# Optimization experiments

Measured on AMD Instinct MI355X. Metric: run time of the kernel, lower is better.

Reference implementation:

```python
import jax, jax.numpy as jnp
import numpy as np

G = 5          # conv groups / adjacency groups
EPS = 1e-5     # BatchNorm eps


def _bn(x, gamma, beta):
    # training-mode BatchNorm2d over (B, J, K) per channel, biased variance
    mean = jnp.mean(x, axis=(0, 2, 3), keepdims=True)
    var = jnp.mean((x - mean) ** 2, axis=(0, 2, 3), keepdims=True)
    xhat = (x - mean) * jax.lax.rsqrt(var + EPS)
    return xhat * gamma[None, :, None, None] + beta[None, :, None, None]


def _xavier(key, shape, fan_in, fan_out):
    a = np.sqrt(6.0 / (fan_in + fan_out))
    return jax.random.uniform(key, shape, jnp.float32, -a, a)


def setup_inputs() -> dict:
    key = jax.random.key(0)
    k0, k1, k2, k3 = jax.random.split(key, 4)
    B, Cin, J, K = 8, 320, 256, 62
    outc = 480
    cin_g, cout_g = Cin // G, outc // G   # 64, 96
    x = jax.random.normal(k0, (B, Cin, J, K), jnp.float32)
    L = jax.random.uniform(k1, (G, K, K), jnp.float32)
    # grouped 1x1 conv weights, stored per-group: [G, out_per_g, in_per_g]
    W1 = _xavier(k2, (G, cout_g, cin_g), cin_g, cout_g)
    W2 = _xavier(k3, (G, cout_g, cout_g), cout_g, cout_g)
    gamma1 = jnp.ones((outc,), jnp.float32)
    beta1 = jnp.zeros((outc,), jnp.float32)
    gamma2 = jnp.ones((outc,), jnp.float32)
    beta2 = jnp.zeros((outc,), jnp.float32)
    return {"x": x, "L": L, "W1": W1, "W2": W2,
            "gamma1": gamma1, "beta1": beta1,
            "gamma2": gamma2, "beta2": beta2}


def reference(x, L, W1, W2, gamma1, beta1, gamma2, beta2):
    B, Cin, J, K = x.shape
    cout_g = W1.shape[1]
    outc = G * cout_g
    # grouped 1x1 conv #1: [B,G,cin_g,J,K] x [G,cout_g,cin_g]
    xg = x.reshape(B, G, Cin // G, J, K)
    h = jnp.einsum('bgcjk,goc->bgojk', xg, W1).reshape(B, outc, J, K)
    h = jax.nn.elu(_bn(h, gamma1, beta1))
    # grouped 1x1 conv #2
    hg = h.reshape(B, G, cout_g, J, K)
    h2 = jnp.einsum('bgcjk,goc->bgojk', hg, W2).reshape(B, outc, J, K)
    h2 = _bn(h2, gamma2, beta2)
    # per-group adjacency einsum: split channels into G groups of cout_g
    y = jnp.einsum('bgijk,gkp->bgijp', h2.reshape(B, G, cout_g, J, K), L)
    return y.reshape(B, outc, J, K)
```

## Files before the change

### kernel.cpp

```cpp
#include <hip/hip_runtime.h>
#include <hip/hip_bf16.h>

#define G 5
#define B 8
#define CIN 320
#define CIN_G 64
#define COUT 480
#define COUT_G 96
#define NPOS 15872
#define NSTAT (B*NPOS)
#define BN_EPS 1e-5f
#define KDIM 62
#define SLABBF 31744

typedef float  f32x4 __attribute__((ext_vector_type(4)));
typedef float  f32x2 __attribute__((ext_vector_type(2)));
typedef __bf16 bf16x8 __attribute__((ext_vector_type(8)));
typedef __bf16 bf16x4 __attribute__((ext_vector_type(4)));

__global__ __launch_bounds__(256) void k_prep(
    const float* __restrict__ W1, const float* __restrict__ W2, const float* __restrict__ L,
    __bf16* __restrict__ W1b, __bf16* __restrict__ W2b, float* __restrict__ lcs)
{
    const int bx = blockIdx.x;
    if (bx < 300) {
        const int i = bx * 256 + threadIdx.x;
        if (i < 30720) W1b[i] = (__bf16)W1[i];
        else W2b[i - 30720] = (__bf16)W2[i - 30720];
    } else {
        const int g = bx - 300, p = threadIdx.x;
        if (p < 64) {
            float s = 0.f;
            if (p < KDIM)
                for (int k = 0; k < KDIM; ++k) s += L[(g * KDIM + k) * KDIM + p];
            lcs[g * 64 + p] = s;
        }
    }
}

__global__ __launch_bounds__(256) void k_stat1(
    const float* __restrict__ x, const __bf16* __restrict__ W1b,
    float* __restrict__ sum1, float* __restrict__ sq1)
{
    __shared__ __bf16 wl[COUT_G * 72];
    __shared__ float st[COUT_G * 2];
    const int b = blockIdx.z, g = blockIdx.y;
    for (int i = threadIdx.x; i < 768; i += 256) {
        const int idx = i * 8, o = idx >> 6, c = idx & 63;
        *(bf16x8*)&wl[o * 72 + c] = *(const bf16x8*)&W1b[g * 6144 + idx];
    }
    if (threadIdx.x < COUT_G * 2) st[threadIdx.x] = 0.f;
    __syncthreads();

    const int wid = threadIdx.x >> 6, lane = threadIdx.x & 63;
    const int lg = lane >> 4, lr = lane & 15;
    const int jw = blockIdx.x * 4 + wid;
    const float* xb = x + ((size_t)b * CIN + g * CIN_G) * NPOS;

    f32x4 acc1[6][4];
#pragma unroll
    for (int mt = 0; mt < 6; ++mt)
#pragma unroll
        for (int nt = 0; nt < 4; ++nt) acc1[mt][nt] = (f32x4){0.f,0.f,0.f,0.f};

#pragma unroll
    for (int ks = 0; ks < 2; ++ks) {
        const int c0 = ks * 32 + lg * 8;
        bf16x8 af[6];
#pragma unroll
        for (int mt = 0; mt < 6; ++mt)
            af[mt] = *(const bf16x8*)&wl[(mt * 16 + lr) * 72 + c0];
#pragma unroll
        for (int nt = 0; nt < 4; ++nt) {
            const int kcol = nt * 16 + lr;
            bf16x8 bfv;
            if (kcol < KDIM) {
                const float* xp = xb + jw * KDIM + kcol;
#pragma unroll
                for (int i = 0; i < 8; ++i) bfv[i] = (__bf16)xp[(size_t)(c0 + i) * NPOS];
            } else {
#pragma unroll
                for (int i = 0; i < 8; ++i) bfv[i] = (__bf16)0.f;
            }
#pragma unroll
            for (int mt = 0; mt < 6; ++mt)
                acc1[mt][nt] = __builtin_amdgcn_mfma_f32_16x16x32_bf16(af[mt], bfv, acc1[mt][nt], 0, 0, 0);
        }
    }

#pragma unroll
    for (int mt = 0; mt < 6; ++mt) {
#pragma unroll
        for (int r = 0; r < 4; ++r) {
            float s = 0.f, q = 0.f;
#pragma unroll
            for (int nt = 0; nt < 4; ++nt) {
                const float v = acc1[mt][nt][r];
                s += v; q += v * v;
            }
#pragma unroll
            for (int m = 1; m <= 8; m <<= 1) {
                s += __shfl_xor(s, m);
                q += __shfl_xor(q, m);
            }
            if (lr == 0) {
                atomicAdd(&st[(mt * 16 + lg * 4 + r) * 2], s);
                atomicAdd(&st[(mt * 16 + lg * 4 + r) * 2 + 1], q);
            }
        }
    }
    __syncthreads();
    if (threadIdx.x < COUT_G) {
        atomicAdd(&sum1[g * COUT_G + threadIdx.x], st[threadIdx.x * 2]);
        atomicAdd(&sq1[g * COUT_G + threadIdx.x], st[threadIdx.x * 2 + 1]);
    }
}

__global__ void k_fin(const float* __restrict__ sum, const float* __restrict__ sq,
                      const float* __restrict__ gamma, const float* __restrict__ beta,
                      float* __restrict__ a, float* __restrict__ bb)
{
    const int ch = blockIdx.x * blockDim.x + threadIdx.x;
    if (ch < COUT) {
        const float invN = 1.f / (float)NSTAT;
        const float mean = sum[ch] * invN;
        const float var  = sq[ch] * invN - mean * mean;
        const float rstd = rsqrtf(var + BN_EPS);
        const float av = gamma[ch] * rstd;
        a[ch]  = av;
        bb[ch] = beta[ch] - mean * av;
    }
}

__global__ __launch_bounds__(256, 2) void k_fused(
    const float* __restrict__ x, const __bf16* __restrict__ W1b, const __bf16* __restrict__ W2b,
    const float* __restrict__ a1, const float* __restrict__ b1,
    __bf16* __restrict__ h2b, float* __restrict__ sum2, float* __restrict__ sq2)
{
    __shared__ __bf16 wl[COUT_G * 72];
    __shared__ __bf16 ht[4 * 6144];
    __shared__ float a1l[96], b1l[96], st[192];
    const int b = blockIdx.z, g = blockIdx.y;
    for (int i = threadIdx.x; i < 768; i += 256) {
        const int idx = i * 8, o = idx >> 6, c = idx & 63;
        *(bf16x8*)&wl[o * 72 + c] = *(const bf16x8*)&W1b[g * 6144 + idx];
    }
    if (threadIdx.x < 96) {
        a1l[threadIdx.x] = a1[g * 96 + threadIdx.x];
        b1l[threadIdx.x] = b1[g * 96 + threadIdx.x];
    }
    if (threadIdx.x < 192) st[threadIdx.x] = 0.f;
    __syncthreads();

    const int wid = threadIdx.x >> 6, lane = threadIdx.x & 63;
    const int lg = lane >> 4, lr = lane & 15;
    const int jw = blockIdx.x * 4 + wid;
    const float* xb = x + ((size_t)b * CIN + g * CIN_G) * NPOS;
    char* htw = (char*)(ht + wid * 6144);

    {
        f32x4 acc1[6][4];
#pragma unroll
        for (int mt = 0; mt < 6; ++mt)
#pragma unroll
            for (int nt = 0; nt < 4; ++nt) acc1[mt][nt] = (f32x4){0.f,0.f,0.f,0.f};

#pragma unroll
        for (int ks = 0; ks < 2; ++ks) {
            const int c0 = ks * 32 + lg * 8;
            bf16x8 af[6];
#pragma unroll
            for (int mt = 0; mt < 6; ++mt)
                af[mt] = *(const bf16x8*)&wl[(mt * 16 + lr) * 72 + c0];
#pragma unroll
            for (int nt = 0; nt < 4; ++nt) {
                const int kcol = nt * 16 + lr;
                bf16x8 bfv;
                if (kcol < KDIM) {
                    const float* xp = xb + jw * KDIM + kcol;
#pragma unroll
                    for (int i = 0; i < 8; ++i) bfv[i] = (__bf16)xp[(size_t)(c0 + i) * NPOS];
                } else {
#pragma unroll
                    for (int i = 0; i < 8; ++i) bfv[i] = (__bf16)0.f;
                }
#pragma unroll
                for (int mt = 0; mt < 6; ++mt)
                    acc1[mt][nt] = __builtin_amdgcn_mfma_f32_16x16x32_bf16(af[mt], bfv, acc1[mt][nt], 0, 0, 0);
            }
        }
#pragma unroll
        for (int mt = 0; mt < 6; ++mt) {
            const int o0 = mt * 16 + lg * 4;
            const int c8 = o0 >> 3;
            const int half = (o0 & 7) >> 2;
#pragma unroll
            for (int nt = 0; nt < 4; ++nt) {
                const int pl = nt * 16 + lr;
                bf16x4 pv;
#pragma unroll
                for (int r = 0; r < 4; ++r) {
                    const int o = o0 + r;
                    float t = a1l[o] * acc1[mt][nt][r] + b1l[o];
                    t = t > 0.f ? t : (__expf(t) - 1.f);
                    pv[r] = (__bf16)t;
                }
                *(bf16x4*)(htw + c8 * 1024 + (pl ^ ((c8 & 3) << 1)) * 16 + half * 8) = pv;
            }
        }
    }

    f32x4 acc2[4][6];
#pragma unroll
    for (int mt = 0; mt < 4; ++mt)
#pragma unroll
        for (int nt = 0; nt < 6; ++nt) acc2[mt][nt] = (f32x4){0.f,0.f,0.f,0.f};

#pragma unroll
    for (int ks = 0; ks < 3; ++ks) {
        const int c0 = ks * 32 + lg * 8;
        const int c8r = ks * 4 + lg;
        bf16x8 a2[4];
#pragma unroll
        for (int mt = 0; mt < 4; ++mt) {
            a2[mt] = *(const bf16x8*)(htw + c8r * 1024 + ((mt * 16 + lr) ^ ((c8r & 3) << 1)) * 16);
            if (mt == 3 && lr >= 14) {
#pragma unroll
                for (int i = 0; i < 8; ++i) a2[mt][i] = (__bf16)0.f;
            }
        }
        bf16x8 bw[6];
#pragma unroll
        for (int nt = 0; nt < 6; ++nt)
            bw[nt] = *(const bf16x8*)&W2b[((size_t)g * 96 + nt * 16 + lr) * 96 + c0];
#pragma unroll
        for (int mt = 0; mt < 4; ++mt)
#pragma unroll
            for (int nt = 0; nt < 6; ++nt)
                acc2[mt][nt] = __builtin_amdgcn_mfma_f32_16x16x32_bf16(a2[mt], bw[nt], acc2[mt][nt], 0, 0, 0);
    }

#pragma unroll
    for (int nt = 0; nt < 6; ++nt) {
        const int o2 = nt * 16 + lr;
        __bf16* sb = h2b + ((size_t)b * COUT + g * 96 + o2) * SLABBF + (size_t)jw * 64;
        float s = 0.f, q = 0.f;
#pragma unroll
        for (int mt = 0; mt < 4; ++mt) {
            bf16x4 pv;
#pragma unroll
            for (int r = 0; r < 4; ++r) {
                const float v = acc2[mt][nt][r];
                s += v; q += v * v;
                pv[r] = (__bf16)v;
            }
            *(bf16x4*)&sb[mt * 16 + lg * 4] = pv;
        }
        s += __shfl_xor(s, 16); q += __shfl_xor(q, 16);
        s += __shfl_xor(s, 32); q += __shfl_xor(q, 32);
        if (lane < 16) {
            atomicAdd(&st[o2 * 2], s);
            atomicAdd(&st[o2 * 2 + 1], q);
        }
    }
    __syncthreads();
    if (threadIdx.x < 96) {
        atomicAdd(&sum2[g * 96 + threadIdx.x], st[threadIdx.x * 2]);
        atomicAdd(&sq2[g * 96 + threadIdx.x], st[threadIdx.x * 2 + 1]);
    }
}

__global__ __launch_bounds__(256) void k_adj(
    float* __restrict__ y, const float* __restrict__ L,
    const float* __restrict__ a2, const float* __restrict__ b2,
    const float* __restrict__ lcs)
{
    __shared__ __bf16 Lt[64 * 72];
    __shared__ float yt[4][32 * KDIM];
    const int ch = blockIdx.x, b = blockIdx.y;
    const int g = ch / COUT_G;
    const int s = b * COUT + ch;
    const float* Lg = L + g * KDIM * KDIM;
    const __bf16* h2b = (const __bf16*)y;

    for (int i = threadIdx.x; i < 4096; i += 256) {
        const int p = i >> 6, k = i & 63;
        Lt[p * 72 + k] = (__bf16)((p < KDIM && k < KDIM) ? Lg[k * KDIM + p] : 0.f);
    }

    const int wid = threadIdx.x >> 6, lane = threadIdx.x & 63;
    const int lg = lane >> 4, lr = lane & 15;
    const int j0 = wid * 64;

    bf16x8 bt[4][2];
#pragma unroll
    for (int nt = 0; nt < 4; ++nt)
#pragma unroll
        for (int ks = 0; ks < 2; ++ks)
            bt[nt][ks] = *(const bf16x8*)&h2b[(size_t)s * SLABBF + (j0 + nt * 16 + lr) * 64 + ks * 32 + lg * 8];
    __syncthreads();

    bf16x8 lt[4][2];
#pragma unroll
    for (int mt = 0; mt < 4; ++mt)
#pragma unroll
        for (int ks = 0; ks < 2; ++ks)
            lt[mt][ks] = *(const bf16x8*)&Lt[(mt * 16 + lr) * 72 + ks * 32 + lg * 8];

    f32x4 acc[4][4];
#pragma unroll
    for (int mt = 0; mt < 4; ++mt)
#pragma unroll
        for (int nt = 0; nt < 4; ++nt) acc[mt][nt] = (f32x4){0.f,0.f,0.f,0.f};

#pragma unroll
    for (int ks = 0; ks < 2; ++ks)
#pragma unroll
        for (int nt = 0; nt < 4; ++nt)
#pragma unroll
            for (int mt = 0; mt < 4; ++mt)
                acc[mt][nt] = __builtin_amdgcn_mfma_f32_16x16x32_bf16(lt[mt][ks], bt[nt][ks], acc[mt][nt], 0, 0, 0);

    const float av = a2[ch], bv = b2[ch];
    f32x4 lcv[4];
#pragma unroll
    for (int mt = 0; mt < 4; ++mt)
        lcv[mt] = *(const f32x4*)&lcs[g * 64 + mt * 16 + lg * 4];

    float* ytw = yt[wid];
#pragma unroll
    for (int half = 0; half < 2; ++half) {
#pragma unroll
        for (int nth = 0; nth < 2; ++nth) {
            const int nt = half * 2 + nth;
            const int row = nth * 16 + lr;
#pragma unroll
            for (int mt = 0; mt < 4; ++mt) {
                const int p0 = mt * 16 + lg * 4;
                f32x2 v0 = { av * acc[mt][nt][0] + bv * lcv[mt][0],
                             av * acc[mt][nt][1] + bv * lcv[mt][1] };
                *(f32x2*)&ytw[row * KDIM + p0] = v0;
                if (p0 < 60) {
                    f32x2 v1 = { av * acc[mt][nt][2] + bv * lcv[mt][2],
                                 av * acc[mt][nt][3] + bv * lcv[mt][3] };
                    *(f32x2*)&ytw[row * KDIM + p0 + 2] = v1;
                }
            }
        }
        float* yg = y + (size_t)s * NPOS + (j0 + half * 32) * KDIM;
#pragma unroll
        for (int it = 0; it < 8; ++it) {
            const int idx = it * 64 + lane;
            if (idx < 496)
                *(f32x4*)&yg[idx * 4] = *(const f32x4*)&ytw[idx * 4];
        }
    }
}

extern "C" void kernel_launch(void* const* d_in, const int* in_sizes, int n_in,
                              void* d_out, int out_size, void* d_ws, size_t ws_size,
                              hipStream_t stream)
{
    const float* x      = (const float*)d_in[0];
    const float* L      = (const float*)d_in[1];
    const float* W1     = (const float*)d_in[2];
    const float* W2     = (const float*)d_in[3];
    const float* gamma1 = (const float*)d_in[4];
    const float* beta1  = (const float*)d_in[5];
    const float* gamma2 = (const float*)d_in[6];
    const float* beta2  = (const float*)d_in[7];
    float* y = (float*)d_out;

    float* ws   = (float*)d_ws;
    float* sum1 = ws;            float* sq1 = ws + 480;
    float* sum2 = ws + 960;      float* sq2 = ws + 1440;
    float* a1   = ws + 1920;     float* b1  = ws + 2400;
    float* a2   = ws + 2880;     float* b2  = ws + 3360;
    float* lcs  = ws + 3840;
    __bf16* W1b = (__bf16*)(ws + 4160);
    __bf16* W2b = (__bf16*)(ws + 19520);

    hipMemsetAsync(ws, 0, 1920 * sizeof(float), stream);

    k_prep <<<305, 256, 0, stream>>>(W1, W2, L, W1b, W2b, lcs);
    k_stat1<<<dim3(64, G, B), 256, 0, stream>>>(x, W1b, sum1, sq1);
    k_fin  <<<2, 256, 0, stream>>>(sum1, sq1, gamma1, beta1, a1, b1);
    k_fused<<<dim3(64, G, B), 256, 0, stream>>>(x, W1b, W2b, a1, b1, (__bf16*)d_out, sum2, sq2);
    k_fin  <<<2, 256, 0, stream>>>(sum2, sq2, gamma2, beta2, a2, b2);
    k_adj  <<<dim3(COUT, B), 256, 0, stream>>>(y, L, a2, b2, lcs);
}
```

Before: 250.6 us.

## Fold BN finalize into consumers and precompute transposed bf16 L in prep

Removes the two tiny k_fin launches by computing the BN scale and shift per channel inside k_fused and k_adj from the accumulated sums. k_prep now also writes a transposed, zero-padded bf16 copy of L to the workspace. k_adj loads its MFMA A-fragments straight from that global copy instead of rebuilding the tile in LDS in every block. This trades launch overhead and redundant per-block transposes for a little repeated arithmetic per block and unpadded global fragment loads.

```diff
diff --git a/kernel.cpp b/kernel.cpp
--- a/kernel.cpp
+++ b/kernel.cpp
@@ -20,7 +20,8 @@
 
 __global__ __launch_bounds__(256) void k_prep(
     const float* __restrict__ W1, const float* __restrict__ W2, const float* __restrict__ L,
-    __bf16* __restrict__ W1b, __bf16* __restrict__ W2b, float* __restrict__ lcs)
+    __bf16* __restrict__ W1b, __bf16* __restrict__ W2b, __bf16* __restrict__ Ltb,
+    float* __restrict__ lcs)
 {
     const int bx = blockIdx.x;
     if (bx < 300) {
@@ -28,12 +29,16 @@
         if (i < 30720) W1b[i] = (__bf16)W1[i];
         else W2b[i - 30720] = (__bf16)W2[i - 30720];
     } else {
-        const int g = bx - 300, p = threadIdx.x;
-        if (p < 64) {
+        const int g = bx - 300;
+        for (int e = threadIdx.x; e < 4096; e += 256) {
+            const int p = e >> 6, k = e & 63;
+            Ltb[g * 4096 + e] = (__bf16)((p < KDIM && k < KDIM) ? L[(g * KDIM + k) * KDIM + p] : 0.f);
+        }
+        if (threadIdx.x < 64) {
             float s = 0.f;
-            if (p < KDIM)
-                for (int k = 0; k < KDIM; ++k) s += L[(g * KDIM + k) * KDIM + p];
-            lcs[g * 64 + p] = s;
+            if (threadIdx.x < KDIM)
+                for (int k = 0; k < KDIM; ++k) s += L[(g * KDIM + k) * KDIM + threadIdx.x];
+            lcs[g * 64 + threadIdx.x] = s;
         }
     }
 }
@@ -116,25 +121,10 @@
     }
 }
 
-__global__ void k_fin(const float* __restrict__ sum, const float* __restrict__ sq,
-                      const float* __restrict__ gamma, const float* __restrict__ beta,
-                      float* __restrict__ a, float* __restrict__ bb)
-{
-    const int ch = blockIdx.x * blockDim.x + threadIdx.x;
-    if (ch < COUT) {
-        const float invN = 1.f / (float)NSTAT;
-        const float mean = sum[ch] * invN;
-        const float var  = sq[ch] * invN - mean * mean;
-        const float rstd = rsqrtf(var + BN_EPS);
-        const float av = gamma[ch] * rstd;
-        a[ch]  = av;
-        bb[ch] = beta[ch] - mean * av;
-    }
-}
-
 __global__ __launch_bounds__(256, 2) void k_fused(
     const float* __restrict__ x, const __bf16* __restrict__ W1b, const __bf16* __restrict__ W2b,
-    const float* __restrict__ a1, const float* __restrict__ b1,
+    const float* __restrict__ sum1, const float* __restrict__ sq1,
+    const float* __restrict__ gamma1, const float* __restrict__ beta1,
     __bf16* __restrict__ h2b, float* __restrict__ sum2, float* __restrict__ sq2)
 {
     __shared__ __bf16 wl[COUT_G * 72];
@@ -146,8 +136,13 @@
         *(bf16x8*)&wl[o * 72 + c] = *(const bf16x8*)&W1b[g * 6144 + idx];
     }
     if (threadIdx.x < 96) {
-        a1l[threadIdx.x] = a1[g * 96 + threadIdx.x];
-        b1l[threadIdx.x] = b1[g * 96 + threadIdx.x];
+        const int ch = g * 96 + threadIdx.x;
+        const float invN = 1.f / (float)NSTAT;
+        const float mean = sum1[ch] * invN;
+        const float var  = sq1[ch] * invN - mean * mean;
+        const float av = gamma1[ch] * rsqrtf(var + BN_EPS);
+        a1l[threadIdx.x] = av;
+        b1l[threadIdx.x] = beta1[ch] - mean * av;
     }
     if (threadIdx.x < 192) st[threadIdx.x] = 0.f;
     __syncthreads();
@@ -271,22 +266,16 @@
 }
 
 __global__ __launch_bounds__(256) void k_adj(
-    float* __restrict__ y, const float* __restrict__ L,
-    const float* __restrict__ a2, const float* __restrict__ b2,
+    float* __restrict__ y, const __bf16* __restrict__ Ltb,
+    const float* __restrict__ sum2, const float* __restrict__ sq2,
+    const float* __restrict__ gamma2, const float* __restrict__ beta2,
     const float* __restrict__ lcs)
 {
-    __shared__ __bf16 Lt[64 * 72];
     __shared__ float yt[4][32 * KDIM];
     const int ch = blockIdx.x, b = blockIdx.y;
     const int g = ch / COUT_G;
     const int s = b * COUT + ch;
-    const float* Lg = L + g * KDIM * KDIM;
     const __bf16* h2b = (const __bf16*)y;
-
-    for (int i = threadIdx.x; i < 4096; i += 256) {
-        const int p = i >> 6, k = i & 63;
-        Lt[p * 72 + k] = (__bf16)((p < KDIM && k < KDIM) ? Lg[k * KDIM + p] : 0.f);
-    }
 
     const int wid = threadIdx.x >> 6, lane = threadIdx.x & 63;
     const int lg = lane >> 4, lr = lane & 15;
@@ -298,14 +287,21 @@
 #pragma unroll
         for (int ks = 0; ks < 2; ++ks)
             bt[nt][ks] = *(const bf16x8*)&h2b[(size_t)s * SLABBF + (j0 + nt * 16 + lr) * 64 + ks * 32 + lg * 8];
-    __syncthreads();
 
     bf16x8 lt[4][2];
 #pragma unroll
     for (int mt = 0; mt < 4; ++mt)
 #pragma unroll
         for (int ks = 0; ks < 2; ++ks)
-            lt[mt][ks] = *(const bf16x8*)&Lt[(mt * 16 + lr) * 72 + ks * 32 + lg * 8];
+            lt[mt][ks] = *(const bf16x8*)&Ltb[g * 4096 + (mt * 16 + lr) * 64 + ks * 32 + lg * 8];
+
+    const float invN = 1.f / (float)NSTAT;
+    const float mean = sum2[ch] * invN;
+    const float var  = sq2[ch] * invN - mean * mean;
+    const float av = gamma2[ch] * rsqrtf(var + BN_EPS);
+    const float bv = beta2[ch] - mean * av;
+
+    __syncthreads();
 
     f32x4 acc[4][4];
 #pragma unroll
@@ -321,7 +317,6 @@
             for (int mt = 0; mt < 4; ++mt)
                 acc[mt][nt] = __builtin_amdgcn_mfma_f32_16x16x32_bf16(lt[mt][ks], bt[nt][ks], acc[mt][nt], 0, 0, 0);
 
-    const float av = a2[ch], bv = b2[ch];
     f32x4 lcv[4];
 #pragma unroll
     for (int mt = 0; mt < 4; ++mt)
@@ -374,18 +369,16 @@
     float* ws   = (float*)d_ws;
     float* sum1 = ws;            float* sq1 = ws + 480;
     float* sum2 = ws + 960;      float* sq2 = ws + 1440;
-    float* a1   = ws + 1920;     float* b1  = ws + 2400;
-    float* a2   = ws + 2880;     float* b2  = ws + 3360;
-    float* lcs  = ws + 3840;
-    __bf16* W1b = (__bf16*)(ws + 4160);
-    __bf16* W2b = (__bf16*)(ws + 19520);
+    float* lcs  = ws + 1920;
+    __bf16* W1b = (__bf16*)(ws + 2240);
+    __bf16* W2b = (__bf16*)(ws + 17600);
+    __bf16* Ltb = (__bf16*)(ws + 40640);
 
     hipMemsetAsync(ws, 0, 1920 * sizeof(float), stream);
 
-    k_prep <<<305, 256, 0, stream>>>(W1, W2, L, W1b, W2b, lcs);
+    k_prep <<<305, 256, 0, stream>>>(W1, W2, L, W1b, W2b, Ltb, lcs);
     k_stat1<<<dim3(64, G, B), 256, 0, stream>>>(x, W1b, sum1, sq1);
-    k_fin  <<<2, 256, 0, stream>>>(sum1, sq1, gamma1, beta1, a1, b1);
-    k_fused<<<dim3(64, G, B), 256, 0, stream>>>(x, W1b, W2b, a1, b1, (__bf16*)d_out, sum2, sq2);
-    k_fin  <<<2, 256, 0, stream>>>(sum2, sq2, gamma2, beta2, a2, b2);
-    k_adj  <<<dim3(COUT, B), 256, 0, stream>>>(y, L, a2, b2, lcs);
-}
+    k_fused<<<dim3(64, G, B), 256, 0, stream>>>(x, W1b, W2b, sum1, sq1, gamma1, beta1,
+                                                (__bf16*)d_out, sum2, sq2);
+    k_adj  <<<dim3(COUT, B), 256, 0, stream>>>(y, Ltb, sum2, sq2, gamma2, beta2, lcs);
+}
```

New measurement: 240.1 us. 4.2% less time.
